# Optimization experiments

Measured on AMD Instinct MI355X. Metric: run time of the kernel, lower is better.

Reference implementation:

```python
import jax, jax.numpy as jnp
import numpy as np

B, S, F, H, T = 1024, 64, 2, 128, 24  # batch, src_len, n_features, hidden, output_length


def setup_inputs() -> dict:
    key = jax.random.key(0)
    ks = jax.random.split(key, 20)
    def p(k, shape):
        return jax.random.normal(k, shape, jnp.float32) * 0.05
    return {
        "x": jax.random.normal(ks[0], (B, S, F), jnp.float32),
        "prev_y": jnp.zeros((B, F), jnp.float32),
        # encoder 3-layer LSTM (PyTorch gate order i,f,g,o; b = b_ih + b_hh fused)
        "enc_Wih0": p(ks[1], (4 * H, F)),
        "enc_Whh0": p(ks[2], (4 * H, H)),
        "enc_b0": p(ks[3], (4 * H,)),
        "enc_Wih12": p(ks[4], (2, 4 * H, H)),
        "enc_Whh12": p(ks[5], (2, 4 * H, H)),
        "enc_b12": p(ks[6], (2, 4 * H)),
        # Bahdanau attention
        "attn_W": p(ks[7], (H, 2 * H)),
        "attn_b": p(ks[8], (H,)),
        "v_W": p(ks[9], (H,)),
        # decoder 3-layer LSTM, input size H+2
        "dec_Wih0": p(ks[10], (4 * H, H + 2)),
        "dec_Whh0": p(ks[11], (4 * H, H)),
        "dec_b0": p(ks[12], (4 * H,)),
        "dec_Wih12": p(ks[13], (2, 4 * H, H)),
        "dec_Whh12": p(ks[14], (2, 4 * H, H)),
        "dec_b12": p(ks[15], (2, 4 * H)),
        # output head Linear(2H, 2)
        "out_W": p(ks[16], (2, 2 * H)),
        "out_b": p(ks[17], (2,)),
    }


def _lstm_cell(xt, h, c, Wih, Whh, b):
    g = xt @ Wih.T + h @ Whh.T + b  # [B, 4H]
    i, f, gg, o = jnp.split(g, 4, axis=-1)
    c = jax.nn.sigmoid(f) * c + jax.nn.sigmoid(i) * jnp.tanh(gg)
    h = jax.nn.sigmoid(o) * jnp.tanh(c)
    return h, c


def _lstm_layer(xs, Wih, Whh, b):
    # xs: [S, B, in] -> hs [S, B, H], final (h, c)
    z = jnp.zeros((xs.shape[1], Whh.shape[1]), xs.dtype)
    def step(carry, xt):
        h, c = _lstm_cell(xt, carry[0], carry[1], Wih, Whh, b)
        return (h, c), h
    (hT, cT), hs = jax.lax.scan(step, (z, z), xs)
    return hs, hT, cT


def reference(x, prev_y, enc_Wih0, enc_Whh0, enc_b0, enc_Wih12, enc_Whh12, enc_b12,
              attn_W, attn_b, v_W, dec_Wih0, dec_Whh0, dec_b0, dec_Wih12, dec_Whh12,
              dec_b12, out_W, out_b):
    # ---- encoder: 3-layer LSTM over time ----
    hs, h0, c0 = _lstm_layer(jnp.swapaxes(x, 0, 1), enc_Wih0, enc_Whh0, enc_b0)
    hid, cel = [h0], [c0]
    for l in range(2):
        hs, hT, cT = _lstm_layer(hs, enc_Wih12[l], enc_Whh12[l], enc_b12[l])
        hid.append(hT); cel.append(cT)
    enc_out = jnp.swapaxes(hs, 0, 1)            # [B, S, H]
    h = jnp.stack(hid)                           # [3, B, H]
    c = jnp.stack(cel)

    def dec_step(carry, _):
        prev_out, h, c = carry
        h_top = h[2]                                             # top-layer hidden [B, H]
        a_in = jnp.concatenate(
            [jnp.broadcast_to(h_top[:, None, :], enc_out.shape), enc_out], axis=-1)  # [B, S, 2H]
        scores = jnp.tanh(a_in @ attn_W.T + attn_b) @ v_W        # [B, S]
        attw = jax.nn.softmax(scores, axis=1)
        weighted = jnp.einsum('bs,bsd->bd', attw, enc_out)        # [B, H]
        rnn_in = jnp.concatenate([prev_out, weighted], axis=-1)   # [B, H+2]
        h0n, c0n = _lstm_cell(rnn_in, h[0], c[0], dec_Wih0, dec_Whh0, dec_b0)
        h1n, c1n = _lstm_cell(h0n, h[1], c[1], dec_Wih12[0], dec_Whh12[0], dec_b12[0])
        h2n, c2n = _lstm_cell(h1n, h[2], c[2], dec_Wih12[1], dec_Whh12[1], dec_b12[1])
        out = jnp.concatenate([h2n, weighted], axis=-1) @ out_W.T + out_b  # [B, 2]
        return (out, jnp.stack([h0n, h1n, h2n]), jnp.stack([c0n, c1n, c2n])), out

    _, outs = jax.lax.scan(dec_step, (prev_y, h, c), None, length=T)
    return outs  # [T, B, 2]
```

## Files before the change

### kernel.cpp

```cpp
#include <hip/hip_runtime.h>
#include <hip/hip_fp16.h>

#define SEQ   64
#define HID   128
#define TOUT  24

typedef unsigned int u32;
typedef _Float16 f16;
typedef __attribute__((ext_vector_type(8))) f16 f16x8;
typedef __attribute__((ext_vector_type(4))) float f32x4;
#define MFMA __builtin_amdgcn_mfma_f32_16x16x32_f16

static __device__ __forceinline__ float sigm(float x){
  return __builtin_amdgcn_rcpf(1.f + __expf(-x));
}
static __device__ __forceinline__ float tanh_fast(float x){
  return fmaf(2.f, __builtin_amdgcn_rcpf(1.f + __expf(-2.f*x)), -1.f);
}

__global__ void prep_kernel(
    const float* __restrict__ eWih0,  const float* __restrict__ eWhh0,
    const float* __restrict__ eWih12, const float* __restrict__ eWhh12,
    const float* __restrict__ aW,
    const float* __restrict__ dWih0,  const float* __restrict__ dWhh0,
    const float* __restrict__ dWih12, const float* __restrict__ dWhh12,
    const float* __restrict__ oW,
    __half* __restrict__ wE0, __half* __restrict__ wE1, __half* __restrict__ wE2,
    __half* __restrict__ wD0, __half* __restrict__ wD1, __half* __restrict__ wD2,
    __half* __restrict__ wAh, __half* __restrict__ wAeF, float* __restrict__ wOT,
    float* __restrict__ dW2)
{
  int id = blockIdx.x*blockDim.x + threadIdx.x;
  if (id < 65536){
    int m=id, jj=m&7, l=(m>>3)&63, kt=(m>>9)&3, nt=m>>11;
    int col = nt*16 + (l&15), k = kt*32 + ((l>>4)<<3) + jj;
    wE0[m] = __float2half(eWhh0[col*128 + k]); return;
  }
  id -= 65536;
  if (id < 5*131072){
    int seg = id >> 17, m = id & 131071;
    int jj=m&7, l=(m>>3)&63, kt=(m>>9)&7, nt=m>>12;
    int col = nt*16 + (l&15), k = kt*32 + ((l>>4)<<3) + jj;
    float v;
    if (seg==0)      v = (k<128)? eWih12[col*128+k]         : eWhh12[col*128 + (k-128)];
    else if (seg==1) v = (k<128)? eWih12[65536+col*128+k]   : eWhh12[65536 + col*128 + (k-128)];
    else if (seg==2) v = (k<128)? dWih0[col*130 + 2 + k]    : dWhh0[col*128 + (k-128)];
    else if (seg==3) v = (k<128)? dWih12[col*128+k]         : dWhh12[col*128 + (k-128)];
    else             v = (k<128)? dWih12[65536+col*128+k]   : dWhh12[65536 + col*128 + (k-128)];
    __half* dst = (seg==0)?wE1:(seg==1)?wE2:(seg==2)?wD0:(seg==3)?wD1:wD2;
    dst[m] = __float2half(v); return;
  }
  id -= 5*131072;
  if (id < 16384){
    int m=id, jj=m&7, l=(m>>3)&63, kt=(m>>9)&3, nt=m>>11;
    int col = nt*16 + (l&15), k = kt*32 + ((l>>4)<<3) + jj;
    wAh[m] = __float2half(aW[col*256 + k]); return;
  }
  id -= 16384;
  if (id < 16384){
    int m=id, jj=m&7, l=(m>>3)&63, kt=(m>>9)&3, nt=m>>11;
    int col = nt*16 + (l&15), k = kt*32 + ((l>>4)<<3) + jj;
    wAeF[m] = __float2half(aW[col*256 + 128 + k]); return;
  }
  id -= 16384;
  if (id < 512){ int k=id>>1, jo=id&1; wOT[id] = oW[jo*256 + k]; return; }
  id -= 512;
  if (id < 1024){ int col=id>>1, ki=id&1; dW2[id] = dWih0[col*130 + ki]; return; }
}

__global__ __launch_bounds__(512) __attribute__((amdgpu_waves_per_eu(2, 2)))
void enc_kernel(
    const float* __restrict__ x, const float* __restrict__ eb0,
    const float* __restrict__ eb12, const float* __restrict__ eWih0,
    const __half* __restrict__ wE0, const __half* __restrict__ wE1,
    const __half* __restrict__ wE2,
    __half* __restrict__ hs0, __half* __restrict__ hs1,
    __half* __restrict__ carryH, float* __restrict__ carryC)
{
  __shared__ __align__(16) __half hT[2][2048];

  const int tid = threadIdx.x, w = tid>>6, lane = tid&63;
  const int l15 = lane&15, g4 = lane>>4;
  const int j = w*16 + l15;
  const int b16 = blockIdx.x*16;
  const int K0 = ((j>>5)*64 + ((j>>3)&3)*16)*8 + (j&7);

  __half* hs0b = hs0 + (size_t)blockIdx.x*131072;
  __half* hs1b = hs1 + (size_t)blockIdx.x*131072;

  for (int layer=0; layer<3; ++layer){
    const __half* W  = (layer==0)? wE0 : (layer==1)? wE1 : wE2;
    const float* bs  = (layer==0)? eb0 : (layer==1)? eb12 : (eb12+512);
    const __half* hinb  = (layer==1)? hs0b : hs1b;
    __half* houtb = (layer==0)? hs0b : (layer==1)? hs1b : nullptr;

    float bias[4];
#pragma unroll
    for (int g=0; g<4; ++g) bias[g] = bs[g*128 + j];
    float2 wx[4];
    if (layer==0){
#pragma unroll
      for (int g=0; g<4; ++g) wx[g] = *(const float2*)(eWih0 + (g*128+j)*2);
    }
    const f16x8* wb = (const f16x8*)W + lane;
    f16x8 Wh[16];
    if (layer==0){
#pragma unroll
      for (int g=0; g<4; ++g)
#pragma unroll
        for (int kt=0; kt<4; ++kt) Wh[g*4+kt] = wb[(size_t)((g*8+w)*4 + kt)*64];
    } else {
#pragma unroll
      for (int g=0; g<4; ++g)
#pragma unroll
        for (int kt=0; kt<4; ++kt) Wh[g*4+kt] = wb[(size_t)((g*8+w)*8 + 4 + kt)*64];
    }
    float c[4] = {0.f,0.f,0.f,0.f};
    ((u32*)hT[0])[tid] = 0u; ((u32*)hT[0])[tid+512] = 0u;
    __syncthreads();

    float2 xv[4]; f16x8 alo[4];
    if (layer==0){
#pragma unroll
      for (int q=0; q<4; ++q) xv[q] = *(const float2*)(x + ((size_t)(b16+g4*4+q)*SEQ + 0)*2);
    } else {
#pragma unroll
      for (int kt=0; kt<4; ++kt) alo[kt] = *(const f16x8*)(hinb + (kt*64+lane)*8);
    }

    int cur = 0;
    for (int t=0; t<SEQ; ++t){
      f16x8 wi[16];
      if (layer>0){
#pragma unroll
        for (int g=0; g<4; ++g)
#pragma unroll
          for (int kt=0; kt<4; ++kt) wi[g*4+kt] = wb[(size_t)((g*8+w)*8 + kt)*64];
      }
      f16x8 ah[4];
#pragma unroll
      for (int kt=0; kt<4; ++kt) ah[kt] = *(const f16x8*)(hT[cur] + (kt*64+lane)*8);
      float2 xcur[4]; f16x8 acur[4];
      if (layer==0){
#pragma unroll
        for (int q=0; q<4; ++q) xcur[q] = xv[q];
        if (t+1 < SEQ)
#pragma unroll
          for (int q=0; q<4; ++q) xv[q] = *(const float2*)(x + ((size_t)(b16+g4*4+q)*SEQ + t+1)*2);
      } else {
#pragma unroll
        for (int kt=0; kt<4; ++kt) acur[kt] = alo[kt];
        if (t+1 < SEQ)
#pragma unroll
          for (int kt=0; kt<4; ++kt) alo[kt] = *(const f16x8*)(hinb + (size_t)(t+1)*2048 + (kt*64+lane)*8);
      }
      f32x4 acc[4];
#pragma unroll
      for (int g=0; g<4; ++g) acc[g] = (f32x4){0.f,0.f,0.f,0.f};
#pragma unroll
      for (int g=0; g<4; ++g)
#pragma unroll
        for (int kt=0; kt<4; ++kt) acc[g] = MFMA(ah[kt], Wh[g*4+kt], acc[g], 0,0,0);
      if (layer>0){
#pragma unroll
        for (int g=0; g<4; ++g)
#pragma unroll
          for (int kt=0; kt<4; ++kt) acc[g] = MFMA(acur[kt], wi[g*4+kt], acc[g], 0,0,0);
      }
#pragma unroll
      for (int q=0; q<4; ++q){
        float gi = acc[0][q]+bias[0], gf = acc[1][q]+bias[1],
              gg = acc[2][q]+bias[2], go = acc[3][q]+bias[3];
        if (layer==0){
          gi += xcur[q].x*wx[0].x + xcur[q].y*wx[0].y;
          gf += xcur[q].x*wx[1].x + xcur[q].y*wx[1].y;
          gg += xcur[q].x*wx[2].x + xcur[q].y*wx[2].y;
          go += xcur[q].x*wx[3].x + xcur[q].y*wx[3].y;
        }
        float cn = fmaf(sigm(gf), c[q], sigm(gi)*tanh_fast(gg));
        float hn = sigm(go)*tanh_fast(cn);
        c[q] = cn;
        __half hh = __float2half(hn);
        hT[cur^1][K0 + (g4*4+q)*8] = hh;
        if (layer < 2){
          houtb[(size_t)t*2048 + K0 + (g4*4+q)*8] = hh;
        } else {
          int off = g4*32768 + q*8192 + (t>>4)*2048 + (j>>5)*512
                  + ((t&15) + ((j>>3)&3)*16)*8 + (j&7);
          hs0b[off] = hh;
        }
        if (t == SEQ-1){
          int ci = (layer*1024 + b16 + g4*4 + q)*128 + j;
          carryH[ci] = hh;
          carryC[ci] = cn;
        }
      }
      __syncthreads();
      cur ^= 1;
    }
    __syncthreads();
  }
}

static __device__ __forceinline__ void dec_gemm(const __half* __restrict__ W,
    const __half* __restrict__ A0, const __half* __restrict__ A1,
    f32x4* acc, int lane, int w)
{
  const f16x8* wb = (const f16x8*)W + (size_t)(8*w)*64 + lane;
  f16x8 q[3][4];
#pragma unroll
  for (int g=0; g<4; ++g) q[0][g] = wb[(size_t)(g*64 + 0)*64];
#pragma unroll
  for (int g=0; g<4; ++g) q[1][g] = wb[(size_t)(g*64 + 1)*64];
  f16x8 a0 = *(const f16x8*)(A0 + lane*8);
#pragma unroll
  for (int g=0; g<4; ++g) acc[g] = (f32x4){0.f,0.f,0.f,0.f};
#pragma unroll
  for (int kt=0; kt<8; ++kt){
    const int cur = kt % 3, nxt = (kt+2) % 3;
    if (kt+2 < 8){
#pragma unroll
      for (int g=0; g<4; ++g) q[nxt][g] = wb[(size_t)(g*64 + kt+2)*64];
    }
    f16x8 a = a0;
    if (kt+1 < 8){
      const __half* An = (kt+1 < 4)? (A0 + (kt+1)*512) : (A1 + (kt-3)*512);
      a0 = *(const f16x8*)(An + lane*8);
    }
#pragma unroll
    for (int g=0; g<4; ++g) acc[g] = MFMA(a, q[cur][g], acc[g], 0,0,0);
  }
}

__global__ __launch_bounds__(512) __attribute__((amdgpu_waves_per_eu(2, 2)))
void dec_kernel(
    const float* __restrict__ prev_y, const float* __restrict__ db0,
    const float* __restrict__ db12, const float* __restrict__ ob,
    const float* __restrict__ ab, const float* __restrict__ vW,
    const __half* __restrict__ wD0, const __half* __restrict__ wD1,
    const __half* __restrict__ wD2, const __half* __restrict__ wAh,
    const __half* __restrict__ wAeF, const float* __restrict__ wOT,
    const float* __restrict__ dW2, const __half* __restrict__ encAg,
    const __half* __restrict__ carryH, const float* __restrict__ carryC,
    float* __restrict__ dout)
{
  __shared__ __align__(16) __half hT[4][2048];
  __shared__ float hp[4][132];
  __shared__ float scbF[256];
  __shared__ __align__(16) __half scb16h[256];
  __shared__ float hw[4*256];
  __shared__ float po[4][2];
  __shared__ float vwl[128];
  extern __shared__ __align__(16) __half dyn[];
  __half* encBL = dyn;
  __half* epL   = dyn + 32768;

  const int tid = threadIdx.x, w = tid>>6, lane = tid&63;
  const int l15 = lane&15, g4 = lane>>4;
  const int j = w*16 + l15;
  const int d = blockIdx.x, b4 = d*4;
  const int K0 = ((j>>5)*64 + ((j>>3)&3)*16)*8 + (j&7);
  const __half* encAd = encAg + (size_t)(d>>2)*131072 + (size_t)(d&3)*32768;

  float cD[3][4];
  if (g4 == 0){
#pragma unroll
    for (int l=0; l<3; ++l)
#pragma unroll
      for (int q=0; q<4; ++q){
        int ci = (l*1024 + b4 + q)*128 + j;
        hT[1+l][K0 + q*8] = carryH[ci];
        cD[l][q] = carryC[ci];
      }
  }
  if (tid < 8) po[tid>>1][tid&1] = prev_y[(b4 + (tid>>1))*2 + (tid&1)];
  if (tid < 128) vwl[tid] = vW[tid];

#pragma unroll
  for (int it=0; it<8; ++it){
    int lin = it*512 + tid;
    f16x8 v = *(const f16x8*)(encAd + (size_t)lin*8);
    int laneA = lin&63, ktA = (lin>>6)&3, sb = (lin>>8)&3, r4 = (lin>>10)&3;
    int s  = sb*16 + (laneA&15);
    int d0 = ktA*32 + ((laneA>>4)<<3);
    int base = r4*8192 + ((d0>>4)*2 + (s>>5))*512 + (s&7);
    int lb0  = (d0&15) + ((s>>3)&3)*16;
    f16* eb = (f16*)encBL;
#pragma unroll
    for (int u=0; u<8; ++u) eb[base + (lb0+u)*8] = v[u];
  }
#pragma unroll
  for (int i=0; i<2; ++i){
    int mt = w*2 + i, r4 = mt>>2, sb = mt&3;
    f16x8 a[4];
#pragma unroll
    for (int kt=0; kt<4; ++kt)
      a[kt] = *(const f16x8*)(encAd + (size_t)(((r4*4+sb)*4 + kt)*64 + lane)*8);
    const f16x8* bw = (const f16x8*)wAeF + lane;
#pragma unroll
    for (int nt=0; nt<8; ++nt){
      int col = nt*16 + l15;
      float abv = ab[col];
      f32x4 acc = {abv, abv, abv, abv};
#pragma unroll
      for (int kt=0; kt<4; ++kt) acc = MFMA(a[kt], bw[(size_t)(nt*4+kt)*64], acc, 0,0,0);
      int srow = r4*64 + sb*16 + g4*4;
#pragma unroll
      for (int q=0; q<4; ++q) epL[(srow+q)*132 + col] = __float2half(acc[q]);
    }
  }
  __syncthreads();

  auto cell = [&](float* crl, const float* bdp, const float* dwp, __half* hdst, float* hwp,
                  const f32x4* acc){
    float b0 = bdp[j], b1 = bdp[128+j], b2 = bdp[256+j], b3 = bdp[384+j];
    float2 w0, w1, w2, w3;
    if (dwp){
      w0 = *(const float2*)(dwp + 2*j);
      w1 = *(const float2*)(dwp + 2*(128+j));
      w2 = *(const float2*)(dwp + 2*(256+j));
      w3 = *(const float2*)(dwp + 2*(384+j));
    }
#pragma unroll
    for (int q=0; q<4; ++q){
      float gi = acc[0][q]+b0, gf = acc[1][q]+b1, gg = acc[2][q]+b2, go = acc[3][q]+b3;
      if (dwp){
        float p0 = po[q][0], p1 = po[q][1];
        gi += p0*w0.x + p1*w0.y;
        gf += p0*w1.x + p1*w1.y;
        gg += p0*w2.x + p1*w2.y;
        go += p0*w3.x + p1*w3.y;
      }
      float cn = fmaf(sigm(gf), crl[q], sigm(gi)*tanh_fast(gg));
      float hn = sigm(go)*tanh_fast(cn);
      crl[q] = cn;
      hdst[K0 + q*8] = __float2half(hn);
      if (hwp) hwp[q*256 + j] = hn;
    }
  };

  int zr = 0;
  for (int t=0; t<TOUT; ++t){
    asm volatile("" : "+v"(zr));
    const float*  db0t  = db0  + zr;
    const float*  db12t = db12 + zr;
    const float*  dW2t  = dW2  + zr;
    const __half* wAht  = wAh  + zr;

    {
      f16x8 a[4], wAhR[4];
      const f16x8* wbh = (const f16x8*)wAht + lane;
#pragma unroll
      for (int kt=0; kt<4; ++kt) wAhR[kt] = wbh[(size_t)(w*4+kt)*64];
#pragma unroll
      for (int kt=0; kt<4; ++kt) a[kt] = *(const f16x8*)(hT[3] + (kt*64+lane)*8);
      f32x4 acc = {0.f,0.f,0.f,0.f};
#pragma unroll
      for (int kt=0; kt<4; ++kt) acc = MFMA(a[kt], wAhR[kt], acc, 0,0,0);
      if (g4 == 0){
#pragma unroll
        for (int q=0; q<4; ++q) hp[q][j] = acc[q];
      }
    }
    __syncthreads();
    {
      int rs = tid>>1, r = rs>>6, jh = tid&1;
      const __half* er = epL + rs*132 + jh*64;
      const float* hr = hp[r] + jh*64;
      const float* vr = vwl + jh*64;
      float sc = 0.f;
#pragma unroll
      for (int p=0; p<8; ++p){
        f16x8 e = *(const f16x8*)(er + p*8);
#pragma unroll
        for (int u=0; u<8; ++u)
          sc = fmaf(tanh_fast((float)e[u] + hr[p*8+u]), vr[p*8+u], sc);
      }
      sc += __shfl_xor(sc, 1);
      if (jh == 0) scbF[rs] = sc;
    }
    __syncthreads();
    if (tid < 256){
      float v = scbF[tid];
      float m = v;
#pragma unroll
      for (int off=32; off; off>>=1) m = fmaxf(m, __shfl_xor(m, off));
      float e = __expf(v - m);
      float sm = e;
#pragma unroll
      for (int off=32; off; off>>=1) sm += __shfl_xor(sm, off);
      scb16h[tid] = __float2half(e * __builtin_amdgcn_rcpf(sm));
    }
    __syncthreads();
    {
#pragma unroll
      for (int r=0; r<4; ++r){
        f32x4 acc = {0.f,0.f,0.f,0.f};
#pragma unroll
        for (int kt=0; kt<2; ++kt){
          f16x8 abc = *(const f16x8*)(scb16h + r*64 + kt*32 + ((lane>>4)<<3));
          f16x8 b   = *(const f16x8*)(encBL + r*8192 + ((w*2+kt)*64 + lane)*8);
          acc = MFMA(abc, b, acc, 0,0,0);
        }
        if (lane < 16){
          hT[0][K0 + r*8] = __float2half(acc[0]);
          hw[r*256 + 128 + j] = acc[0];
        }
      }
    }
    __syncthreads();
    f32x4 acc[4];
    dec_gemm(wD0, hT[0], hT[1], acc, lane, w);
    __syncthreads();
    if (g4 == 0) cell(cD[0], db0t, dW2t, hT[1], nullptr, acc);
    __syncthreads();
    dec_gemm(wD1, hT[1], hT[2], acc, lane, w);
    __syncthreads();
    if (g4 == 0) cell(cD[1], db12t, nullptr, hT[2], nullptr, acc);
    __syncthreads();
    dec_gemm(wD2, hT[2], hT[3], acc, lane, w);
    __syncthreads();
    if (g4 == 0) cell(cD[2], db12t + 512, nullptr, hT[3], hw, acc);
    __syncthreads();
    if (tid < 128){
      int r = tid>>5, kl = tid&31;
      float o0 = 0.f, o1 = 0.f;
#pragma unroll
      for (int i=0; i<8; ++i){
        int k = kl*8 + i;
        float hv = hw[r*256 + k];
        float2 wv = *(const float2*)(wOT + k*2);
        o0 = fmaf(hv, wv.x, o0); o1 = fmaf(hv, wv.y, o1);
      }
#pragma unroll
      for (int off=16; off; off>>=1){ o0 += __shfl_xor(o0, off); o1 += __shfl_xor(o1, off); }
      if (kl == 0){
        float v0 = o0 + ob[0], v1 = o1 + ob[1];
        size_t oi = ((size_t)t*1024 + b4 + r)*2;
        dout[oi] = v0; dout[oi+1] = v1;
        po[r][0] = v0; po[r][1] = v1;
      }
    }
    __syncthreads();
  }
}

extern "C" void kernel_launch(void* const* d_in, const int* in_sizes, int n_in,
                              void* d_out, int out_size, void* d_ws, size_t ws_size,
                              hipStream_t stream) {
  const float* x      = (const float*)d_in[0];
  const float* prev_y = (const float*)d_in[1];
  const float* eWih0  = (const float*)d_in[2];
  const float* eWhh0  = (const float*)d_in[3];
  const float* eb0    = (const float*)d_in[4];
  const float* eWih12 = (const float*)d_in[5];
  const float* eWhh12 = (const float*)d_in[6];
  const float* eb12   = (const float*)d_in[7];
  const float* aW     = (const float*)d_in[8];
  const float* ab     = (const float*)d_in[9];
  const float* vW     = (const float*)d_in[10];
  const float* dWih0  = (const float*)d_in[11];
  const float* dWhh0  = (const float*)d_in[12];
  const float* db0    = (const float*)d_in[13];
  const float* dWih12 = (const float*)d_in[14];
  const float* dWhh12 = (const float*)d_in[15];
  const float* db12   = (const float*)d_in[16];
  const float* oW     = (const float*)d_in[17];
  const float* ob     = (const float*)d_in[18];

  __half* wE0  = (__half*)d_ws;
  __half* wE1  = wE0 + 65536;
  __half* wE2  = wE1 + 131072;
  __half* wD0  = wE2 + 131072;
  __half* wD1  = wD0 + 131072;
  __half* wD2  = wD1 + 131072;
  __half* wAh  = wD2 + 131072;
  __half* wAeF = wAh + 16384;
  float*  wOT  = (float*)(wAeF + 16384);
  float*  dW2  = wOT + 512;
  __half* hs0  = (__half*)(dW2 + 1024);
  __half* hs1  = hs0 + (size_t)64*131072;
  __half* carryH = hs1 + (size_t)64*131072;
  float*  carryC = (float*)(carryH + 393216);

  const int prepN = 65536 + 5*131072 + 16384 + 16384 + 512 + 1024;
  prep_kernel<<<(prepN + 255)/256, 256, 0, stream>>>(
      eWih0, eWhh0, eWih12, eWhh12, aW, dWih0, dWhh0, dWih12, dWhh12, oW,
      wE0, wE1, wE2, wD0, wD1, wD2, wAh, wAeF, wOT, dW2);

  enc_kernel<<<64, 512, 0, stream>>>(
      x, eb0, eb12, eWih0, wE0, wE1, wE2, hs0, hs1, carryH, carryC);

  const int dynB = (32768 + 256*132) * 2;
  hipFuncSetAttribute(reinterpret_cast<const void*>(dec_kernel),
                      hipFuncAttributeMaxDynamicSharedMemorySize, dynB);
  dec_kernel<<<256, 512, dynB, stream>>>(
      prev_y, db0, db12, ob, ab, vW, wD0, wD1, wD2, wAh, wAeF, wOT, dW2,
      hs0, carryH, carryC, (float*)d_out);
}
```

Before: 616.1 us.

## Restructure decoder GEMM prefetch by gate and stagger wave-to-column mapping per block

The decoder GEMM now loads all eight A fragments into registers up front and streams weights gate by gate in groups of four k-tiles. The next gate's weights are fetched while the current gate's four MFMAs run, replacing the per-k-tile triple-buffered loop. Each block also rotates which hidden-column slice a wave owns (w8 = (w+d)&7), so concurrent blocks read different weight rows at the same moment and L2/channel hot spots are spread out. This raises register pressure from the larger in-flight buffers, and it only works if every column-dependent index uses w8 consistently.

```diff
diff --git a/kernel.cpp b/kernel.cpp
--- a/kernel.cpp
+++ b/kernel.cpp
@@ -202,34 +202,41 @@
   }
 }
 
+#define LDQ(Q, g, kh) \
+  Q[0] = wb[(size_t)((g)*64 + (kh)*4 + 0)*64]; \
+  Q[1] = wb[(size_t)((g)*64 + (kh)*4 + 1)*64]; \
+  Q[2] = wb[(size_t)((g)*64 + (kh)*4 + 2)*64]; \
+  Q[3] = wb[(size_t)((g)*64 + (kh)*4 + 3)*64];
+#define MM4(Q, A, g) \
+  acc[g] = MFMA(A[0], Q[0], acc[g], 0,0,0); \
+  acc[g] = MFMA(A[1], Q[1], acc[g], 0,0,0); \
+  acc[g] = MFMA(A[2], Q[2], acc[g], 0,0,0); \
+  acc[g] = MFMA(A[3], Q[3], acc[g], 0,0,0);
+
 static __device__ __forceinline__ void dec_gemm(const __half* __restrict__ W,
     const __half* __restrict__ A0, const __half* __restrict__ A1,
-    f32x4* acc, int lane, int w)
+    f32x4* acc, int lane, int w8)
 {
-  const f16x8* wb = (const f16x8*)W + (size_t)(8*w)*64 + lane;
-  f16x8 q[3][4];
-#pragma unroll
-  for (int g=0; g<4; ++g) q[0][g] = wb[(size_t)(g*64 + 0)*64];
-#pragma unroll
-  for (int g=0; g<4; ++g) q[1][g] = wb[(size_t)(g*64 + 1)*64];
-  f16x8 a0 = *(const f16x8*)(A0 + lane*8);
+  const f16x8* wb = (const f16x8*)W + (size_t)(w8*8)*64 + lane;
+  f16x8 q0[4], q1[4], q2[4], q3[4];
+  f16x8 a0[4], a1[4];
+  LDQ(q0, 0, 0)
+  LDQ(q1, 1, 0)
+  LDQ(q2, 2, 0)
+#pragma unroll
+  for (int kt=0; kt<4; ++kt) a0[kt] = *(const f16x8*)(A0 + (kt*64+lane)*8);
 #pragma unroll
   for (int g=0; g<4; ++g) acc[g] = (f32x4){0.f,0.f,0.f,0.f};
-#pragma unroll
-  for (int kt=0; kt<8; ++kt){
-    const int cur = kt % 3, nxt = (kt+2) % 3;
-    if (kt+2 < 8){
-#pragma unroll
-      for (int g=0; g<4; ++g) q[nxt][g] = wb[(size_t)(g*64 + kt+2)*64];
-    }
-    f16x8 a = a0;
-    if (kt+1 < 8){
-      const __half* An = (kt+1 < 4)? (A0 + (kt+1)*512) : (A1 + (kt-3)*512);
-      a0 = *(const f16x8*)(An + lane*8);
-    }
-#pragma unroll
-    for (int g=0; g<4; ++g) acc[g] = MFMA(a, q[cur][g], acc[g], 0,0,0);
-  }
+  MM4(q0, a0, 0)  LDQ(q3, 3, 0)
+  MM4(q1, a0, 1)  LDQ(q0, 0, 1)
+#pragma unroll
+  for (int kt=0; kt<4; ++kt) a1[kt] = *(const f16x8*)(A1 + (kt*64+lane)*8);
+  MM4(q2, a0, 2)  LDQ(q1, 1, 1)
+  MM4(q3, a0, 3)  LDQ(q2, 2, 1)
+  MM4(q0, a1, 0)  LDQ(q3, 3, 1)
+  MM4(q1, a1, 1)
+  MM4(q2, a1, 2)
+  MM4(q3, a1, 3)
 }
 
 __global__ __launch_bounds__(512) __attribute__((amdgpu_waves_per_eu(2, 2)))
@@ -257,8 +264,9 @@
 
   const int tid = threadIdx.x, w = tid>>6, lane = tid&63;
   const int l15 = lane&15, g4 = lane>>4;
-  const int j = w*16 + l15;
   const int d = blockIdx.x, b4 = d*4;
+  const int w8 = (w + d) & 7;
+  const int j = w8*16 + l15;
   const int K0 = ((j>>5)*64 + ((j>>3)&3)*16)*8 + (j&7);
   const __half* encAd = encAg + (size_t)(d>>2)*131072 + (size_t)(d&3)*32768;
 
@@ -351,7 +359,7 @@
       f16x8 a[4], wAhR[4];
       const f16x8* wbh = (const f16x8*)wAht + lane;
 #pragma unroll
-      for (int kt=0; kt<4; ++kt) wAhR[kt] = wbh[(size_t)(w*4+kt)*64];
+      for (int kt=0; kt<4; ++kt) wAhR[kt] = wbh[(size_t)(w8*4+kt)*64];
 #pragma unroll
       for (int kt=0; kt<4; ++kt) a[kt] = *(const f16x8*)(hT[3] + (kt*64+lane)*8);
       f32x4 acc = {0.f,0.f,0.f,0.f};
@@ -399,7 +407,7 @@
 #pragma unroll
         for (int kt=0; kt<2; ++kt){
           f16x8 abc = *(const f16x8*)(scb16h + r*64 + kt*32 + ((lane>>4)<<3));
-          f16x8 b   = *(const f16x8*)(encBL + r*8192 + ((w*2+kt)*64 + lane)*8);
+          f16x8 b   = *(const f16x8*)(encBL + r*8192 + ((w8*2+kt)*64 + lane)*8);
           acc = MFMA(abc, b, acc, 0,0,0);
         }
         if (lane < 16){
@@ -410,15 +418,15 @@
     }
     __syncthreads();
     f32x4 acc[4];
-    dec_gemm(wD0, hT[0], hT[1], acc, lane, w);
+    dec_gemm(wD0, hT[0], hT[1], acc, lane, w8);
     __syncthreads();
     if (g4 == 0) cell(cD[0], db0t, dW2t, hT[1], nullptr, acc);
     __syncthreads();
-    dec_gemm(wD1, hT[1], hT[2], acc, lane, w);
+    dec_gemm(wD1, hT[1], hT[2], acc, lane, w8);
     __syncthreads();
     if (g4 == 0) cell(cD[1], db12t, nullptr, hT[2], nullptr, acc);
     __syncthreads();
-    dec_gemm(wD2, hT[2], hT[3], acc, lane, w);
+    dec_gemm(wD2, hT[2], hT[3], acc, lane, w8);
     __syncthreads();
     if (g4 == 0) cell(cD[2], db12t + 512, nullptr, hT[3], hw, acc);
     __syncthreads();
```

New measurement: 624.2 us. About the same (+1.3%).
